# Optimization experiments

Hardware: AMD Instinct MI355X
Metric: run time of the kernel (lower is better)

## Reference

```python
import jax, jax.numpy as jnp
import numpy as np

# Classifier3Stage core of Reg_3stage (giga_depth), defaults: close_far_separation=False, c3_line_div=1
BS, CIN, H, W = 1, 128, 112, 320
CL = (16, 16, 16)          # classes per stage
PAD = (0, 8, 8)
C12 = CL[0] * CL[1]        # 256
C123 = C12 * CL[2]         # 4096
C1D = [128, 32, 32, CL[0] + 2 * PAD[0]]   # per-line grouped conv dims: 128->32->32->16
C2D = [128, 32, 32, CL[1] + 2 * PAD[1]]   # CondMul stage2 dims: 128->32->32->32
C3D = [128, 32, 32, CL[2] + 2 * PAD[2]]   # CondMul stage3 dims (in=ch_latent[0][i], out=ch_latent[1][i+1])


def setup_inputs() -> dict:
    key = jax.random.key(0)

    def p(i, shape):
        return jax.random.normal(jax.random.fold_in(key, i), shape, jnp.float32) * 0.05

    d = {"x_in": jax.random.normal(jax.random.fold_in(key, 0), (BS, CIN, H, W), jnp.float32)}
    for i in range(3):  # c1: per-line (grouped) 1x1 convs -> [H, out, in] weights
        d[f"w1_{i}"] = p(10 + 2 * i, (H, C1D[i + 1], C1D[i]))
        d[f"b1_{i}"] = p(11 + 2 * i, (H, C1D[i + 1]))
    for i in range(3):  # c2: CondMul over H*classes0 conditions
        d[f"w2_{i}"] = p(20 + 2 * i, (H * CL[0], C2D[i], C2D[i + 1]))
        d[f"b2_{i}"] = p(21 + 2 * i, (H * CL[0], C2D[i + 1]))
    for i in range(3):  # c3: CondMul over H*classes12 conditions
        d[f"w3_{i}"] = p(30 + 2 * i, (H * C12, C3D[i], C3D[i + 1]))
        d[f"b3_{i}"] = p(31 + 2 * i, (H * C12, C3D[i + 1]))
    return d


def _lrelu(v):
    return jnp.where(v >= 0, v, 0.01 * v)


def _condmul(x, inds, w, b):
    # x: [N, Cin], inds: [N] int32, w: [K, Cin, Cout], b: [K, Cout]
    return jnp.einsum('ni,nio->no', x, w[inds]) + b[inds]


def reference(x_in, w1_0, b1_0, w1_1, b1_1, w1_2, b1_2,
              w2_0, b2_0, w2_1, b2_1, w2_2, b2_2,
              w3_0, b3_0, w3_1, b3_1, w3_2, b3_2):
    bs, C, h, w = x_in.shape
    x = jnp.transpose(x_in, (0, 2, 3, 1))              # [bs,H,W,C] (far segment = x_in, per-line layout)
    # stage 1: per-line 1x1 grouped convs
    t = x
    for (wt, bt, last) in [(w1_0, b1_0, False), (w1_1, b1_1, False), (w1_2, b1_2, True)]:
        t = jnp.einsum('bhwi,hoi->bhwo', t, wt) + bt[None, :, None, :]
        if not last:
            t = _lrelu(t)
    inds1 = jnp.argmax(t, axis=-1).astype(jnp.int32)   # [bs,H,W]
    off = jnp.arange(h, dtype=jnp.int32)[None, :, None]
    x_l = x.reshape(-1, C)                             # rows in (b,h,w) order
    i1l = (inds1 + CL[0] * off).reshape(-1)
    # stage 2: CondMul chain routed by line*class1 index
    y = _lrelu(_condmul(x_l, i1l, w2_0, b2_0))
    y = _lrelu(_condmul(y, i1l, w2_1, b2_1))
    y = _condmul(y, i1l, w2_2, b2_2)                   # [N, 32]
    inds2 = jnp.argmax(y, axis=1).astype(jnp.int32).reshape(bs, h, w)
    inds12 = inds1 * CL[1] + (inds2 - PAD[1])
    i12l = (jnp.clip(inds12, 0, C12 - 1) + C12 * off).reshape(-1)  # c3_line_div=1 -> scaled == unscaled
    # stage 3: CondMul chain routed by line*classes12 index (close segment = x_in)
    z = _lrelu(_condmul(x_l, i12l, w3_0, b3_0))
    z = _lrelu(_condmul(z, i12l, w3_1, b3_1))
    z = _condmul(z, i12l, w3_2, b3_2)                  # [N, 32]
    inds3 = jnp.argmax(z, axis=1).astype(jnp.int32).reshape(bs, h, w)
    inds123 = jnp.clip(inds12 * CL[2] + (inds3 - PAD[2]), 0, C123 - 1)
    return inds123.reshape(bs, 1, h, w)
```

## Files before the change

### kernel.cpp

```cpp
#include <hip/hip_runtime.h>

#define HH   112
#define WW   320
#define CIN_ 128
#define HW_  (HH * WW)
#define CHUNK 32

__device__ __forceinline__ float lrelu(float v) {
    return v >= 0.f ? v : 0.01f * v;
}

__global__ __launch_bounds__(512, 2)
void k1_stage1(const float* __restrict__ x_in,
               const float* __restrict__ w1_0, const float* __restrict__ b1_0,
               const float* __restrict__ w1_1, const float* __restrict__ b1_1,
               const float* __restrict__ w1_2, const float* __restrict__ b1_2,
               int* __restrict__ inds1_out, float* __restrict__ xT_out,
               int* __restrict__ qc2, int* __restrict__ qc3)
{
    __shared__ float w1s0[32][CIN_ + 1];
    __shared__ float w1s1[32][33];
    __shared__ float w1s2[16][33];
    __shared__ float b1s[80];
    __shared__ float xT[16][132];

    const int h   = blockIdx.x >> 2;
    const int q   = blockIdx.x & 3;
    const int tid = threadIdx.x;
    const int base = h * WW;

    if (blockIdx.x == 0 && tid == 0) { *qc2 = 0; *qc3 = 0; }

    for (int n = tid; n < 32 * CIN_; n += 512)
        w1s0[n >> 7][n & 127] = w1_0[h * (32 * CIN_) + n];
    for (int n = tid; n < 32 * 32; n += 512)
        w1s1[n >> 5][n & 31] = w1_1[h * 1024 + n];
    if (tid < 16 * 32)
        w1s2[tid >> 5][tid & 31] = w1_2[h * 512 + tid];
    if      (tid < 32) b1s[tid] = b1_0[h * 32 + tid];
    else if (tid < 64) b1s[tid] = b1_1[h * 32 + (tid - 32)];
    else if (tid < 80) b1s[tid] = b1_2[h * 16 + (tid - 64)];
    __syncthreads();

    const int wave = tid >> 6;
    const int lane = tid & 63;
    const int o    = lane & 31;
    const int half = lane >> 5;
    const int o16  = lane & 15;

    for (int t = 0; t < 5; ++t) {
        const int w0 = q * 80 + t * 16;
        for (int n = tid; n < 16 * CIN_; n += 512) {
            int ww = n & 15, c = n >> 4;
            xT[ww][c] = x_in[c * HW_ + base + w0 + ww];
        }
        __syncthreads();
        for (int n = tid; n < 16 * CIN_; n += 512) {
            int pix = n >> 7, c = n & 127;
            xT_out[(size_t)(base + w0 + pix) * CIN_ + c] = xT[pix][c];
        }
        const float* xA = &xT[wave][0];
        const float* xB = &xT[wave + 8][0];

        float aA = 0.f, aB = 0.f;
        #pragma unroll
        for (int i = 0; i < 64; i += 4) {
            const int ii = half * 64 + i;
            const float w0v = w1s0[o][ii];
            const float w1v = w1s0[o][ii + 1];
            const float w2v = w1s0[o][ii + 2];
            const float w3v = w1s0[o][ii + 3];
            const float4 a4 = *reinterpret_cast<const float4*>(&xA[ii]);
            const float4 b4 = *reinterpret_cast<const float4*>(&xB[ii]);
            aA += a4.x * w0v;  aB += b4.x * w0v;
            aA += a4.y * w1v;  aB += b4.y * w1v;
            aA += a4.z * w2v;  aB += b4.z * w2v;
            aA += a4.w * w3v;  aB += b4.w * w3v;
        }
        aA += __shfl_xor(aA, 32);
        aB += __shfl_xor(aB, 32);
        float yA = lrelu(aA + b1s[o]);
        float yB = lrelu(aB + b1s[o]);

        aA = 0.f; aB = 0.f;
        #pragma unroll
        for (int i = 0; i < 32; ++i) {
            const float wv = w1s1[o][i];
            aA += __shfl(yA, i) * wv;
            aB += __shfl(yB, i) * wv;
        }
        float y2A = lrelu(aA + b1s[32 + o]);
        float y2B = lrelu(aB + b1s[32 + o]);

        aA = 0.f; aB = 0.f;
        #pragma unroll
        for (int i = 0; i < 32; ++i) {
            const float wv = w1s2[o16][i];
            aA += __shfl(y2A, i) * wv;
            aB += __shfl(y2B, i) * wv;
        }
        const float t1A = aA + b1s[64 + o16];
        const float t1B = aB + b1s[64 + o16];

        float bvA = t1A, bvB = t1B;
        int   biA = o16, biB = o16;
        #pragma unroll
        for (int d = 1; d < 16; d <<= 1) {
            float ovA = __shfl_xor(bvA, d), ovB = __shfl_xor(bvB, d);
            int   oiA = __shfl_xor(biA, d), oiB = __shfl_xor(biB, d);
            if (ovA > bvA || (ovA == bvA && oiA < biA)) { bvA = ovA; biA = oiA; }
            if (ovB > bvB || (ovB == bvB && oiB < biB)) { bvB = ovB; biB = oiB; }
        }
        if (lane == 0) {
            inds1_out[base + w0 + wave]     = biA;
            inds1_out[base + w0 + wave + 8] = biB;
        }
        __syncthreads();
    }
}

template <int BINS>
__global__ void sorter(const int* __restrict__ inds_in, int clipmax,
                       int* __restrict__ sorted, int4* __restrict__ queue,
                       int* __restrict__ qcount)
{
    __shared__ int cnt[BINS];
    __shared__ int scan[BINS];
    __shared__ int rank[BINS];

    const int h = blockIdx.x, tid = threadIdx.x, base = h * WW;
    if (tid < BINS) { cnt[tid] = 0; rank[tid] = 0; }
    __syncthreads();

    int c = -1;
    if (tid < WW) {
        c = inds_in[base + tid];
        c = min(max(c, 0), clipmax);
        atomicAdd(&cnt[c], 1);
    }
    __syncthreads();
    if (tid < BINS) scan[tid] = cnt[tid];
    __syncthreads();
    for (int s = 1; s < BINS; s <<= 1) {
        int v = 0;
        if (tid >= s && tid < BINS) v = scan[tid - s];
        __syncthreads();
        if (tid < BINS) scan[tid] += v;
        __syncthreads();
    }
    if (tid < WW) {
        int pos = (scan[c] - cnt[c]) + atomicAdd(&rank[c], 1);
        sorted[base + pos] = base + tid;
    }
    if (tid < BINS && cnt[tid] > 0) {
        int offc = scan[tid] - cnt[tid];
        for (int s0 = 0; s0 < cnt[tid]; s0 += CHUNK) {
            int qi = atomicAdd(qcount, 1);
            queue[qi] = make_int4(h, tid, base + offc + s0,
                                  min(CHUNK, cnt[tid] - s0));
        }
    }
}

#define COMPUTE_ROUND(TB, PA, PB, PC, PD)                                      \
{                                                                              \
    float a0 = 0.f, a1 = 0.f, a2 = 0.f, a3 = 0.f;                              \
    _Pragma("unroll")                                                          \
    for (int i = 0; i < 64; i += 4) {                                          \
        const int ii = half * 64 + i;                                          \
        const float w0v = ws0[(ii + 0) * 32 + o];                              \
        const float w1v = ws0[(ii + 1) * 32 + o];                              \
        const float w2v = ws0[(ii + 2) * 32 + o];                              \
        const float w3v = ws0[(ii + 3) * 32 + o];                              \
        const float4 v0 = *reinterpret_cast<const float4*>(&xbuf[wave*4+0][ii]);\
        const float4 v1 = *reinterpret_cast<const float4*>(&xbuf[wave*4+1][ii]);\
        const float4 v2 = *reinterpret_cast<const float4*>(&xbuf[wave*4+2][ii]);\
        const float4 v3 = *reinterpret_cast<const float4*>(&xbuf[wave*4+3][ii]);\
        a0 += v0.x * w0v; a1 += v1.x * w0v; a2 += v2.x * w0v; a3 += v3.x * w0v;\
        a0 += v0.y * w1v; a1 += v1.y * w1v; a2 += v2.y * w1v; a3 += v3.y * w1v;\
        a0 += v0.z * w2v; a1 += v1.z * w2v; a2 += v2.z * w2v; a3 += v3.z * w2v;\
        a0 += v0.w * w3v; a1 += v1.w * w3v; a2 += v2.w * w3v; a3 += v3.w * w3v;\
    }                                                                          \
    a0 += __shfl_xor(a0, 32); a1 += __shfl_xor(a1, 32);                        \
    a2 += __shfl_xor(a2, 32); a3 += __shfl_xor(a3, 32);                        \
    ys[wave][0][o] = lrelu(a0 + bs[o]);                                        \
    ys[wave][1][o] = lrelu(a1 + bs[o]);                                        \
    ys[wave][2][o] = lrelu(a2 + bs[o]);                                        \
    ys[wave][3][o] = lrelu(a3 + bs[o]);                                        \
    a0 = a1 = a2 = a3 = 0.f;                                                   \
    _Pragma("unroll")                                                          \
    for (int i = 0; i < 32; i += 4) {                                          \
        const float w0v = ws1[(i + 0) * 32 + o];                               \
        const float w1v = ws1[(i + 1) * 32 + o];                               \
        const float w2v = ws1[(i + 2) * 32 + o];                               \
        const float w3v = ws1[(i + 3) * 32 + o];                               \
        const float4 y0 = *reinterpret_cast<const float4*>(&ys[wave][0][i]);   \
        const float4 y1 = *reinterpret_cast<const float4*>(&ys[wave][1][i]);   \
        const float4 y2 = *reinterpret_cast<const float4*>(&ys[wave][2][i]);   \
        const float4 y3 = *reinterpret_cast<const float4*>(&ys[wave][3][i]);   \
        a0 += y0.x * w0v; a1 += y1.x * w0v; a2 += y2.x * w0v; a3 += y3.x * w0v;\
        a0 += y0.y * w1v; a1 += y1.y * w1v; a2 += y2.y * w1v; a3 += y3.y * w1v;\
        a0 += y0.z * w2v; a1 += y1.z * w2v; a2 += y2.z * w2v; a3 += y3.z * w2v;\
        a0 += y0.w * w3v; a1 += y1.w * w3v; a2 += y2.w * w3v; a3 += y3.w * w3v;\
    }                                                                          \
    ys[wave][0][o] = lrelu(a0 + bs[32 + o]);                                   \
    ys[wave][1][o] = lrelu(a1 + bs[32 + o]);                                   \
    ys[wave][2][o] = lrelu(a2 + bs[32 + o]);                                   \
    ys[wave][3][o] = lrelu(a3 + bs[32 + o]);                                   \
    a0 = a1 = a2 = a3 = 0.f;                                                   \
    _Pragma("unroll")                                                          \
    for (int i = 0; i < 32; i += 4) {                                          \
        const float w0v = ws2[(i + 0) * 32 + o];                               \
        const float w1v = ws2[(i + 1) * 32 + o];                               \
        const float w2v = ws2[(i + 2) * 32 + o];                               \
        const float w3v = ws2[(i + 3) * 32 + o];                               \
        const float4 y0 = *reinterpret_cast<const float4*>(&ys[wave][0][i]);   \
        const float4 y1 = *reinterpret_cast<const float4*>(&ys[wave][1][i]);   \
        const float4 y2 = *reinterpret_cast<const float4*>(&ys[wave][2][i]);   \
        const float4 y3 = *reinterpret_cast<const float4*>(&ys[wave][3][i]);   \
        a0 += y0.x * w0v; a1 += y1.x * w0v; a2 += y2.x * w0v; a3 += y3.x * w0v;\
        a0 += y0.y * w1v; a1 += y1.y * w1v; a2 += y2.y * w1v; a3 += y3.y * w1v;\
        a0 += y0.z * w2v; a1 += y1.z * w2v; a2 += y2.z * w2v; a3 += y3.z * w2v;\
        a0 += y0.w * w3v; a1 += y1.w * w3v; a2 += y2.w * w3v; a3 += y3.w * w3v;\
    }                                                                          \
    float bv0 = a0 + bs[64 + o], bv1 = a1 + bs[64 + o];                        \
    float bv2 = a2 + bs[64 + o], bv3 = a3 + bs[64 + o];                        \
    int bi0 = o, bi1 = o, bi2 = o, bi3 = o;                                    \
    _Pragma("unroll")                                                          \
    for (int d = 1; d < 32; d <<= 1) {                                         \
        const float ov0 = __shfl_xor(bv0, d); const int oi0 = __shfl_xor(bi0, d);\
        const float ov1 = __shfl_xor(bv1, d); const int oi1 = __shfl_xor(bi1, d);\
        const float ov2 = __shfl_xor(bv2, d); const int oi2 = __shfl_xor(bi2, d);\
        const float ov3 = __shfl_xor(bv3, d); const int oi3 = __shfl_xor(bi3, d);\
        if (ov0 > bv0 || (ov0 == bv0 && oi0 < bi0)) { bv0 = ov0; bi0 = oi0; }  \
        if (ov1 > bv1 || (ov1 == bv1 && oi1 < bi1)) { bv1 = ov1; bi1 = oi1; }  \
        if (ov2 > bv2 || (ov2 == bv2 && oi2 < bi2)) { bv2 = ov2; bi2 = oi2; }  \
        if (ov3 > bv3 || (ov3 == bv3 && oi3 < bi3)) { bv3 = ov3; bi3 = oi3; }  \
    }                                                                          \
    if (lane == 0) {                                                           \
        const int tb4 = (TB) + wave * 4;                                       \
        if (STAGE == 2) {                                                      \
            if (tb4 + 0 < n) result[PA] = c * 16 + bi0 - 8;                    \
            if (tb4 + 1 < n) result[PB] = c * 16 + bi1 - 8;                    \
            if (tb4 + 2 < n) result[PC] = c * 16 + bi2 - 8;                    \
            if (tb4 + 3 < n) result[PD] = c * 16 + bi3 - 8;                    \
        } else {                                                               \
            if (tb4 + 0 < n) result[PA] = min(max(inds12_in[PA] * 16 + bi0 - 8, 0), 4095); \
            if (tb4 + 1 < n) result[PB] = min(max(inds12_in[PB] * 16 + bi1 - 8, 0), 4095); \
            if (tb4 + 2 < n) result[PC] = min(max(inds12_in[PC] * 16 + bi2 - 8, 0), 4095); \
            if (tb4 + 3 < n) result[PD] = min(max(inds12_in[PD] * 16 + bi3 - 8, 0), 4095); \
        }                                                                      \
    }                                                                          \
}

template <int STAGE>
__global__ __launch_bounds__(256, 4)
void qk_compute(const float* __restrict__ xT_in, const int* __restrict__ sorted,
                const int4* __restrict__ queue, const int* __restrict__ qcount,
                const float* __restrict__ W0, const float* __restrict__ Bb0,
                const float* __restrict__ W1, const float* __restrict__ Bb1,
                const float* __restrict__ W2, const float* __restrict__ Bb2,
                const int* __restrict__ inds12_in, int* __restrict__ result)
{
    __shared__ float ws0[CIN_ * 32];
    __shared__ float ws1[32 * 32];
    __shared__ float ws2[32 * 32];
    __shared__ float bs[96];
    __shared__ float xbuf[16][CIN_];
    __shared__ float ys[4][4][32];

    const int tid  = threadIdx.x;
    const int wave = tid >> 6;
    const int lane = tid & 63;
    const int o    = lane & 31;
    const int half = lane >> 5;

    const int qn = *qcount;
    for (int qi = blockIdx.x; qi < qn; qi += gridDim.x) {
        const int4 it4   = queue[qi];
        const int  c     = it4.y;
        const int  start = it4.z;
        const int  n     = it4.w;
        const int  key   = (STAGE == 2) ? (it4.x * 16 + c) : (it4.x * 256 + c);
        const int  nr    = (n + 15) >> 4;
        const int  t0    = wave * 4;

        __syncthreads();

        const int pA0 = sorted[start + min(t0 + 0, n - 1)];
        const int pB0 = sorted[start + min(t0 + 1, n - 1)];
        const int pC0 = sorted[start + min(t0 + 2, n - 1)];
        const int pD0 = sorted[start + min(t0 + 3, n - 1)];
        const float2 xA0 = *reinterpret_cast<const float2*>(&xT_in[(size_t)pA0 * CIN_ + 2 * lane]);
        const float2 xB0 = *reinterpret_cast<const float2*>(&xT_in[(size_t)pB0 * CIN_ + 2 * lane]);
        const float2 xC0 = *reinterpret_cast<const float2*>(&xT_in[(size_t)pC0 * CIN_ + 2 * lane]);
        const float2 xD0 = *reinterpret_cast<const float2*>(&xT_in[(size_t)pD0 * CIN_ + 2 * lane]);

        for (int i = tid; i < 1024; i += 256)
            ((float4*)ws0)[i] = ((const float4*)(W0 + (size_t)key * 4096))[i];
        ((float4*)ws1)[tid] = ((const float4*)(W1 + (size_t)key * 1024))[tid];
        ((float4*)ws2)[tid] = ((const float4*)(W2 + (size_t)key * 1024))[tid];
        if      (tid < 32) bs[tid] = Bb0[(size_t)key * 32 + tid];
        else if (tid < 64) bs[tid] = Bb1[(size_t)key * 32 + (tid - 32)];
        else if (tid < 96) bs[tid] = Bb2[(size_t)key * 32 + (tid - 64)];
        __syncthreads();

        *reinterpret_cast<float2*>(&xbuf[wave * 4 + 0][2 * lane]) = xA0;
        *reinterpret_cast<float2*>(&xbuf[wave * 4 + 1][2 * lane]) = xB0;
        *reinterpret_cast<float2*>(&xbuf[wave * 4 + 2][2 * lane]) = xC0;
        *reinterpret_cast<float2*>(&xbuf[wave * 4 + 3][2 * lane]) = xD0;

        int pA1 = 0, pB1 = 0, pC1 = 0, pD1 = 0;
        float2 xA1 = {0.f, 0.f}, xB1 = {0.f, 0.f}, xC1 = {0.f, 0.f}, xD1 = {0.f, 0.f};
        if (nr == 2) {
            pA1 = sorted[start + min(16 + t0 + 0, n - 1)];
            pB1 = sorted[start + min(16 + t0 + 1, n - 1)];
            pC1 = sorted[start + min(16 + t0 + 2, n - 1)];
            pD1 = sorted[start + min(16 + t0 + 3, n - 1)];
            xA1 = *reinterpret_cast<const float2*>(&xT_in[(size_t)pA1 * CIN_ + 2 * lane]);
            xB1 = *reinterpret_cast<const float2*>(&xT_in[(size_t)pB1 * CIN_ + 2 * lane]);
            xC1 = *reinterpret_cast<const float2*>(&xT_in[(size_t)pC1 * CIN_ + 2 * lane]);
            xD1 = *reinterpret_cast<const float2*>(&xT_in[(size_t)pD1 * CIN_ + 2 * lane]);
        }

        COMPUTE_ROUND(0, pA0, pB0, pC0, pD0)

        if (nr == 2) {
            *reinterpret_cast<float2*>(&xbuf[wave * 4 + 0][2 * lane]) = xA1;
            *reinterpret_cast<float2*>(&xbuf[wave * 4 + 1][2 * lane]) = xB1;
            *reinterpret_cast<float2*>(&xbuf[wave * 4 + 2][2 * lane]) = xC1;
            *reinterpret_cast<float2*>(&xbuf[wave * 4 + 3][2 * lane]) = xD1;
            COMPUTE_ROUND(16, pA1, pB1, pC1, pD1)
        }
    }
}

__global__ __launch_bounds__(512, 4)
void reg3_fused(const float* __restrict__ x_in,
                const float* __restrict__ w1_0, const float* __restrict__ b1_0,
                const float* __restrict__ w1_1, const float* __restrict__ b1_1,
                const float* __restrict__ w1_2, const float* __restrict__ b1_2,
                const float* __restrict__ w2_0, const float* __restrict__ b2_0,
                const float* __restrict__ w2_1, const float* __restrict__ b2_1,
                const float* __restrict__ w2_2, const float* __restrict__ b2_2,
                const float* __restrict__ w3_0, const float* __restrict__ b3_0,
                const float* __restrict__ w3_1, const float* __restrict__ b3_1,
                const float* __restrict__ w3_2, const float* __restrict__ b3_2,
                int* __restrict__ out)
{
    __shared__ float xT[8][CIN_ + 1];
    __shared__ float w1s0[32][CIN_ + 1];
    __shared__ float w1s1[32][33];
    __shared__ float w1s2[16][33];
    __shared__ float b1s[80];

    const int h   = blockIdx.x / 40;
    const int w0  = (blockIdx.x % 40) * 8;
    const int tid = threadIdx.x;

    for (int n = tid; n < 8 * CIN_; n += 512) {
        int ww = n & 7, c = n >> 3;
        xT[ww][c] = x_in[c * HW_ + h * WW + w0 + ww];
    }
    for (int n = tid; n < 32 * CIN_; n += 512)
        w1s0[n >> 7][n & 127] = w1_0[h * (32 * CIN_) + n];
    for (int n = tid; n < 32 * 32; n += 512)
        w1s1[n >> 5][n & 31] = w1_1[h * 1024 + n];
    if (tid < 16 * 32)
        w1s2[tid >> 5][tid & 31] = w1_2[h * 512 + tid];
    if      (tid < 32) b1s[tid] = b1_0[h * 32 + tid];
    else if (tid < 64) b1s[tid] = b1_1[h * 32 + (tid - 32)];
    else if (tid < 80) b1s[tid] = b1_2[h * 16 + (tid - 64)];
    __syncthreads();

    const int wave = tid >> 6, lane = tid & 63;
    const int o = lane & 31, half = lane >> 5, o16 = lane & 15;
    const float* xr = &xT[wave][0];

    float acc = 0.f;
    #pragma unroll
    for (int i = 0; i < 64; ++i) { int ii = half * 64 + i; acc += xr[ii] * w1s0[o][ii]; }
    acc += __shfl_xor(acc, 32);
    float y = lrelu(acc + b1s[o]);
    acc = 0.f;
    #pragma unroll
    for (int i = 0; i < 32; ++i) acc += __shfl(y, i) * w1s1[o][i];
    float y2 = lrelu(acc + b1s[32 + o]);
    acc = 0.f;
    #pragma unroll
    for (int i = 0; i < 32; ++i) acc += __shfl(y2, i) * w1s2[o16][i];
    float t1 = acc + b1s[64 + o16];

    float bv = t1; int bi = o16;
    #pragma unroll
    for (int d = 1; d < 16; d <<= 1) {
        float ov = __shfl_xor(bv, d); int oi = __shfl_xor(bi, d);
        if (ov > bv || (ov == bv && oi < bi)) { bv = ov; bi = oi; }
    }
    const int inds1 = bi;
    const int idx1  = inds1 + 16 * h;

    const float* Wp = w2_0 + (size_t)idx1 * (CIN_ * 32);
    acc = 0.f;
    #pragma unroll
    for (int i = 0; i < 64; ++i) { int ii = half * 64 + i; acc += xr[ii] * Wp[ii * 32 + o]; }
    acc += __shfl_xor(acc, 32);
    y = lrelu(acc + b2_0[idx1 * 32 + o]);
    Wp = w2_1 + (size_t)idx1 * 1024;
    acc = 0.f;
    #pragma unroll
    for (int i = 0; i < 32; ++i) acc += __shfl(y, i) * Wp[i * 32 + o];
    y2 = lrelu(acc + b2_1[idx1 * 32 + o]);
    Wp = w2_2 + (size_t)idx1 * 1024;
    acc = 0.f;
    #pragma unroll
    for (int i = 0; i < 32; ++i) acc += __shfl(y2, i) * Wp[i * 32 + o];
    float y3 = acc + b2_2[idx1 * 32 + o];

    bv = y3; bi = o;
    #pragma unroll
    for (int d = 1; d < 32; d <<= 1) {
        float ov = __shfl_xor(bv, d); int oi = __shfl_xor(bi, d);
        if (ov > bv || (ov == bv && oi < bi)) { bv = ov; bi = oi; }
    }
    const int inds2  = bi;
    const int inds12 = inds1 * 16 + inds2 - 8;
    const int clip12 = min(max(inds12, 0), 255);
    const int idx12  = clip12 + 256 * h;

    Wp = w3_0 + (size_t)idx12 * (CIN_ * 32);
    acc = 0.f;
    #pragma unroll
    for (int i = 0; i < 64; ++i) { int ii = half * 64 + i; acc += xr[ii] * Wp[ii * 32 + o]; }
    acc += __shfl_xor(acc, 32);
    y = lrelu(acc + b3_0[idx12 * 32 + o]);
    Wp = w3_1 + (size_t)idx12 * 1024;
    acc = 0.f;
    #pragma unroll
    for (int i = 0; i < 32; ++i) acc += __shfl(y, i) * Wp[i * 32 + o];
    y2 = lrelu(acc + b3_1[idx12 * 32 + o]);
    Wp = w3_2 + (size_t)idx12 * 1024;
    acc = 0.f;
    #pragma unroll
    for (int i = 0; i < 32; ++i) acc += __shfl(y2, i) * Wp[i * 32 + o];
    y3 = acc + b3_2[idx12 * 32 + o];

    bv = y3; bi = o;
    #pragma unroll
    for (int d = 1; d < 32; d <<= 1) {
        float ov = __shfl_xor(bv, d); int oi = __shfl_xor(bi, d);
        if (ov > bv || (ov == bv && oi < bi)) { bv = ov; bi = oi; }
    }
    int inds123 = inds12 * 16 + bi - 8;
    inds123 = min(max(inds123, 0), 4095);
    if (lane == 0) out[h * WW + w0 + wave] = inds123;
}

extern "C" void kernel_launch(void* const* d_in, const int* in_sizes, int n_in,
                              void* d_out, int out_size, void* d_ws, size_t ws_size,
                              hipStream_t stream)
{
    const float* x_in = (const float*)d_in[0];
    const float* w1_0 = (const float*)d_in[1];
    const float* b1_0 = (const float*)d_in[2];
    const float* w1_1 = (const float*)d_in[3];
    const float* b1_1 = (const float*)d_in[4];
    const float* w1_2 = (const float*)d_in[5];
    const float* b1_2 = (const float*)d_in[6];
    const float* w2_0 = (const float*)d_in[7];
    const float* b2_0 = (const float*)d_in[8];
    const float* w2_1 = (const float*)d_in[9];
    const float* b2_1 = (const float*)d_in[10];
    const float* w2_2 = (const float*)d_in[11];
    const float* b2_2 = (const float*)d_in[12];
    const float* w3_0 = (const float*)d_in[13];
    const float* b3_0 = (const float*)d_in[14];
    const float* w3_1 = (const float*)d_in[15];
    const float* b3_1 = (const float*)d_in[16];
    const float* w3_2 = (const float*)d_in[17];
    const float* b3_2 = (const float*)d_in[18];
    int* out = (int*)d_out;

    char* ws = (char*)d_ws;
    int*   inds1_ws  = (int*)(ws + 0);
    int*   inds12_ws = (int*)(ws + 143360);
    int*   sorted2   = (int*)(ws + 286720);
    int*   sorted3   = (int*)(ws + 430080);
    int*   qc2       = (int*)(ws + 573440);
    int*   qc3       = (int*)(ws + 573444);
    int4*  queue2    = (int4*)(ws + 573456);
    int4*  queue3    = (int4*)(ws + 1146896);
    float* xT_ws     = (float*)(ws + 1720336);
    const size_t NEED = 1720336 + (size_t)HW_ * CIN_ * 4;

    if (ws_size >= NEED) {
        k1_stage1<<<HH * 4, 512, 0, stream>>>(
            x_in, w1_0, b1_0, w1_1, b1_1, w1_2, b1_2,
            inds1_ws, xT_ws, qc2, qc3);
        sorter<16><<<HH, 512, 0, stream>>>(inds1_ws, 15, sorted2, queue2, qc2);
        qk_compute<2><<<2048, 256, 0, stream>>>(
            xT_ws, sorted2, queue2, qc2,
            w2_0, b2_0, w2_1, b2_1, w2_2, b2_2, nullptr, inds12_ws);
        sorter<256><<<HH, 512, 0, stream>>>(inds12_ws, 255, sorted3, queue3, qc3);
        qk_compute<3><<<2048, 256, 0, stream>>>(
            xT_ws, sorted3, queue3, qc3,
            w3_0, b3_0, w3_1, b3_1, w3_2, b3_2, inds12_ws, out);
    } else {
        reg3_fused<<<HH * 40, 512, 0, stream>>>(
            x_in, w1_0, b1_0, w1_1, b1_1, w1_2, b1_2,
            w2_0, b2_0, w2_1, b2_1, w2_2, b2_2,
            w3_0, b3_0, w3_1, b3_1, w3_2, b3_2, out);
    }
}
```

Baseline: 200.0 us.

## Use single-wave work items reading condmul weights directly from global memory

The queue kernels now run one 64-thread wave per block with chunks of 8 pixels instead of 256-thread blocks with chunks of 32. Weights and biases are read straight from global memory (through cache) rather than staged in shared memory, which removes the block-wide barriers and the cost of staging a full weight set for small buckets. Per-item weight staging and barrier overhead go away, at the cost of more queue items and more global or L2 weight traffic when a bucket spans several chunks. The waitcnt plus sched_barrier stands in for the dropped __syncthreads, since each item is now handled by a single wave.

Result: slower. 231.1 us (+15.5%).

```diff
diff --git a/kernel.cpp b/kernel.cpp
--- a/kernel.cpp
+++ b/kernel.cpp
@@ -4,7 +4,7 @@
 #define WW   320
 #define CIN_ 128
 #define HW_  (HH * WW)
-#define CHUNK 32
+#define CHUNK 8
 
 __device__ __forceinline__ float lrelu(float v) {
     return v >= 0.f ? v : 0.01f * v;
@@ -162,20 +162,20 @@
     }
 }
 
-#define COMPUTE_ROUND(TB, PA, PB, PC, PD)                                      \
+#define COMPUTE_ROUND(TB, RB, PA, PB, PC, PD)                                  \
 {                                                                              \
     float a0 = 0.f, a1 = 0.f, a2 = 0.f, a3 = 0.f;                              \
     _Pragma("unroll")                                                          \
     for (int i = 0; i < 64; i += 4) {                                          \
         const int ii = half * 64 + i;                                          \
-        const float w0v = ws0[(ii + 0) * 32 + o];                              \
-        const float w1v = ws0[(ii + 1) * 32 + o];                              \
-        const float w2v = ws0[(ii + 2) * 32 + o];                              \
-        const float w3v = ws0[(ii + 3) * 32 + o];                              \
-        const float4 v0 = *reinterpret_cast<const float4*>(&xbuf[wave*4+0][ii]);\
-        const float4 v1 = *reinterpret_cast<const float4*>(&xbuf[wave*4+1][ii]);\
-        const float4 v2 = *reinterpret_cast<const float4*>(&xbuf[wave*4+2][ii]);\
-        const float4 v3 = *reinterpret_cast<const float4*>(&xbuf[wave*4+3][ii]);\
+        const float w0v = Wg0[(ii + 0) * 32 + o];                              \
+        const float w1v = Wg0[(ii + 1) * 32 + o];                              \
+        const float w2v = Wg0[(ii + 2) * 32 + o];                              \
+        const float w3v = Wg0[(ii + 3) * 32 + o];                              \
+        const float4 v0 = *reinterpret_cast<const float4*>(&xbuf[(RB) + 0][ii]);\
+        const float4 v1 = *reinterpret_cast<const float4*>(&xbuf[(RB) + 1][ii]);\
+        const float4 v2 = *reinterpret_cast<const float4*>(&xbuf[(RB) + 2][ii]);\
+        const float4 v3 = *reinterpret_cast<const float4*>(&xbuf[(RB) + 3][ii]);\
         a0 += v0.x * w0v; a1 += v1.x * w0v; a2 += v2.x * w0v; a3 += v3.x * w0v;\
         a0 += v0.y * w1v; a1 += v1.y * w1v; a2 += v2.y * w1v; a3 += v3.y * w1v;\
         a0 += v0.z * w2v; a1 += v1.z * w2v; a2 += v2.z * w2v; a3 += v3.z * w2v;\
@@ -183,48 +183,48 @@
     }                                                                          \
     a0 += __shfl_xor(a0, 32); a1 += __shfl_xor(a1, 32);                        \
     a2 += __shfl_xor(a2, 32); a3 += __shfl_xor(a3, 32);                        \
-    ys[wave][0][o] = lrelu(a0 + bs[o]);                                        \
-    ys[wave][1][o] = lrelu(a1 + bs[o]);                                        \
-    ys[wave][2][o] = lrelu(a2 + bs[o]);                                        \
-    ys[wave][3][o] = lrelu(a3 + bs[o]);                                        \
+    ys[0][o] = lrelu(a0 + b0v);                                                \
+    ys[1][o] = lrelu(a1 + b0v);                                                \
+    ys[2][o] = lrelu(a2 + b0v);                                                \
+    ys[3][o] = lrelu(a3 + b0v);                                                \
     a0 = a1 = a2 = a3 = 0.f;                                                   \
     _Pragma("unroll")                                                          \
     for (int i = 0; i < 32; i += 4) {                                          \
-        const float w0v = ws1[(i + 0) * 32 + o];                               \
-        const float w1v = ws1[(i + 1) * 32 + o];                               \
-        const float w2v = ws1[(i + 2) * 32 + o];                               \
-        const float w3v = ws1[(i + 3) * 32 + o];                               \
-        const float4 y0 = *reinterpret_cast<const float4*>(&ys[wave][0][i]);   \
-        const float4 y1 = *reinterpret_cast<const float4*>(&ys[wave][1][i]);   \
-        const float4 y2 = *reinterpret_cast<const float4*>(&ys[wave][2][i]);   \
-        const float4 y3 = *reinterpret_cast<const float4*>(&ys[wave][3][i]);   \
+        const float w0v = Wg1[(i + 0) * 32 + o];                               \
+        const float w1v = Wg1[(i + 1) * 32 + o];                               \
+        const float w2v = Wg1[(i + 2) * 32 + o];                               \
+        const float w3v = Wg1[(i + 3) * 32 + o];                               \
+        const float4 y0 = *reinterpret_cast<const float4*>(&ys[0][i]);         \
+        const float4 y1 = *reinterpret_cast<const float4*>(&ys[1][i]);         \
+        const float4 y2 = *reinterpret_cast<const float4*>(&ys[2][i]);         \
+        const float4 y3 = *reinterpret_cast<const float4*>(&ys[3][i]);         \
         a0 += y0.x * w0v; a1 += y1.x * w0v; a2 += y2.x * w0v; a3 += y3.x * w0v;\
         a0 += y0.y * w1v; a1 += y1.y * w1v; a2 += y2.y * w1v; a3 += y3.y * w1v;\
         a0 += y0.z * w2v; a1 += y1.z * w2v; a2 += y2.z * w2v; a3 += y3.z * w2v;\
         a0 += y0.w * w3v; a1 += y1.w * w3v; a2 += y2.w * w3v; a3 += y3.w * w3v;\
     }                                                                          \
-    ys[wave][0][o] = lrelu(a0 + bs[32 + o]);                                   \
-    ys[wave][1][o] = lrelu(a1 + bs[32 + o]);                                   \
-    ys[wave][2][o] = lrelu(a2 + bs[32 + o]);                                   \
-    ys[wave][3][o] = lrelu(a3 + bs[32 + o]);                                   \
+    ys[0][o] = lrelu(a0 + b1v);                                                \
+    ys[1][o] = lrelu(a1 + b1v);                                                \
+    ys[2][o] = lrelu(a2 + b1v);                                                \
+    ys[3][o] = lrelu(a3 + b1v);                                                \
     a0 = a1 = a2 = a3 = 0.f;                                                   \
     _Pragma("unroll")                                                          \
     for (int i = 0; i < 32; i += 4) {                                          \
-        const float w0v = ws2[(i + 0) * 32 + o];                               \
-        const float w1v = ws2[(i + 1) * 32 + o];                               \
-        const float w2v = ws2[(i + 2) * 32 + o];                               \
-        const float w3v = ws2[(i + 3) * 32 + o];                               \
-        const float4 y0 = *reinterpret_cast<const float4*>(&ys[wave][0][i]);   \
-        const float4 y1 = *reinterpret_cast<const float4*>(&ys[wave][1][i]);   \
-        const float4 y2 = *reinterpret_cast<const float4*>(&ys[wave][2][i]);   \
-        const float4 y3 = *reinterpret_cast<const float4*>(&ys[wave][3][i]);   \
+        const float w0v = Wg2[(i + 0) * 32 + o];                               \
+        const float w1v = Wg2[(i + 1) * 32 + o];                               \
+        const float w2v = Wg2[(i + 2) * 32 + o];                               \
+        const float w3v = Wg2[(i + 3) * 32 + o];                               \
+        const float4 y0 = *reinterpret_cast<const float4*>(&ys[0][i]);         \
+        const float4 y1 = *reinterpret_cast<const float4*>(&ys[1][i]);         \
+        const float4 y2 = *reinterpret_cast<const float4*>(&ys[2][i]);         \
+        const float4 y3 = *reinterpret_cast<const float4*>(&ys[3][i]);         \
         a0 += y0.x * w0v; a1 += y1.x * w0v; a2 += y2.x * w0v; a3 += y3.x * w0v;\
         a0 += y0.y * w1v; a1 += y1.y * w1v; a2 += y2.y * w1v; a3 += y3.y * w1v;\
         a0 += y0.z * w2v; a1 += y1.z * w2v; a2 += y2.z * w2v; a3 += y3.z * w2v;\
         a0 += y0.w * w3v; a1 += y1.w * w3v; a2 += y2.w * w3v; a3 += y3.w * w3v;\
     }                                                                          \
-    float bv0 = a0 + bs[64 + o], bv1 = a1 + bs[64 + o];                        \
-    float bv2 = a2 + bs[64 + o], bv3 = a3 + bs[64 + o];                        \
+    float bv0 = a0 + b2v, bv1 = a1 + b2v;                                      \
+    float bv2 = a2 + b2v, bv3 = a3 + b2v;                                      \
     int bi0 = o, bi1 = o, bi2 = o, bi3 = o;                                    \
     _Pragma("unroll")                                                          \
     for (int d = 1; d < 32; d <<= 1) {                                         \
@@ -238,23 +238,22 @@
         if (ov3 > bv3 || (ov3 == bv3 && oi3 < bi3)) { bv3 = ov3; bi3 = oi3; }  \
     }                                                                          \
     if (lane == 0) {                                                           \
-        const int tb4 = (TB) + wave * 4;                                       \
         if (STAGE == 2) {                                                      \
-            if (tb4 + 0 < n) result[PA] = c * 16 + bi0 - 8;                    \
-            if (tb4 + 1 < n) result[PB] = c * 16 + bi1 - 8;                    \
-            if (tb4 + 2 < n) result[PC] = c * 16 + bi2 - 8;                    \
-            if (tb4 + 3 < n) result[PD] = c * 16 + bi3 - 8;                    \
+            if ((TB) + 0 < n) result[PA] = c * 16 + bi0 - 8;                   \
+            if ((TB) + 1 < n) result[PB] = c * 16 + bi1 - 8;                   \
+            if ((TB) + 2 < n) result[PC] = c * 16 + bi2 - 8;                   \
+            if ((TB) + 3 < n) result[PD] = c * 16 + bi3 - 8;                   \
         } else {                                                               \
-            if (tb4 + 0 < n) result[PA] = min(max(inds12_in[PA] * 16 + bi0 - 8, 0), 4095); \
-            if (tb4 + 1 < n) result[PB] = min(max(inds12_in[PB] * 16 + bi1 - 8, 0), 4095); \
-            if (tb4 + 2 < n) result[PC] = min(max(inds12_in[PC] * 16 + bi2 - 8, 0), 4095); \
-            if (tb4 + 3 < n) result[PD] = min(max(inds12_in[PD] * 16 + bi3 - 8, 0), 4095); \
+            if ((TB) + 0 < n) result[PA] = min(max(inds12_in[PA] * 16 + bi0 - 8, 0), 4095); \
+            if ((TB) + 1 < n) result[PB] = min(max(inds12_in[PB] * 16 + bi1 - 8, 0), 4095); \
+            if ((TB) + 2 < n) result[PC] = min(max(inds12_in[PC] * 16 + bi2 - 8, 0), 4095); \
+            if ((TB) + 3 < n) result[PD] = min(max(inds12_in[PD] * 16 + bi3 - 8, 0), 4095); \
         }                                                                      \
     }                                                                          \
 }
 
 template <int STAGE>
-__global__ __launch_bounds__(256, 4)
+__global__ __launch_bounds__(64, 4)
 void qk_compute(const float* __restrict__ xT_in, const int* __restrict__ sorted,
                 const int4* __restrict__ queue, const int* __restrict__ qcount,
                 const float* __restrict__ W0, const float* __restrict__ Bb0,
@@ -262,16 +261,10 @@
                 const float* __restrict__ W2, const float* __restrict__ Bb2,
                 const int* __restrict__ inds12_in, int* __restrict__ result)
 {
-    __shared__ float ws0[CIN_ * 32];
-    __shared__ float ws1[32 * 32];
-    __shared__ float ws2[32 * 32];
-    __shared__ float bs[96];
-    __shared__ float xbuf[16][CIN_];
-    __shared__ float ys[4][4][32];
-
-    const int tid  = threadIdx.x;
-    const int wave = tid >> 6;
-    const int lane = tid & 63;
+    __shared__ float xbuf[8][CIN_];
+    __shared__ float ys[4][32];
+
+    const int lane = threadIdx.x;
     const int o    = lane & 31;
     const int half = lane >> 5;
 
@@ -282,55 +275,45 @@
         const int  start = it4.z;
         const int  n     = it4.w;
         const int  key   = (STAGE == 2) ? (it4.x * 16 + c) : (it4.x * 256 + c);
-        const int  nr    = (n + 15) >> 4;
-        const int  t0    = wave * 4;
-
-        __syncthreads();
-
-        const int pA0 = sorted[start + min(t0 + 0, n - 1)];
-        const int pB0 = sorted[start + min(t0 + 1, n - 1)];
-        const int pC0 = sorted[start + min(t0 + 2, n - 1)];
-        const int pD0 = sorted[start + min(t0 + 3, n - 1)];
+
+        const float* __restrict__ Wg0 = W0 + (size_t)key * 4096;
+        const float* __restrict__ Wg1 = W1 + (size_t)key * 1024;
+        const float* __restrict__ Wg2 = W2 + (size_t)key * 1024;
+        const float b0v = Bb0[(size_t)key * 32 + o];
+        const float b1v = Bb1[(size_t)key * 32 + o];
+        const float b2v = Bb2[(size_t)key * 32 + o];
+
+        const int pA0 = sorted[start + min(0, n - 1)];
+        const int pB0 = sorted[start + min(1, n - 1)];
+        const int pC0 = sorted[start + min(2, n - 1)];
+        const int pD0 = sorted[start + min(3, n - 1)];
+        const int pA1 = sorted[start + min(4, n - 1)];
+        const int pB1 = sorted[start + min(5, n - 1)];
+        const int pC1 = sorted[start + min(6, n - 1)];
+        const int pD1 = sorted[start + min(7, n - 1)];
         const float2 xA0 = *reinterpret_cast<const float2*>(&xT_in[(size_t)pA0 * CIN_ + 2 * lane]);
         const float2 xB0 = *reinterpret_cast<const float2*>(&xT_in[(size_t)pB0 * CIN_ + 2 * lane]);
         const float2 xC0 = *reinterpret_cast<const float2*>(&xT_in[(size_t)pC0 * CIN_ + 2 * lane]);
         const float2 xD0 = *reinterpret_cast<const float2*>(&xT_in[(size_t)pD0 * CIN_ + 2 * lane]);
-
-        for (int i = tid; i < 1024; i += 256)
-            ((float4*)ws0)[i] = ((const float4*)(W0 + (size_t)key * 4096))[i];
-        ((float4*)ws1)[tid] = ((const float4*)(W1 + (size_t)key * 1024))[tid];
-        ((float4*)ws2)[tid] = ((const float4*)(W2 + (size_t)key * 1024))[tid];
-        if      (tid < 32) bs[tid] = Bb0[(size_t)key * 32 + tid];
-        else if (tid < 64) bs[tid] = Bb1[(size_t)key * 32 + (tid - 32)];
-        else if (tid < 96) bs[tid] = Bb2[(size_t)key * 32 + (tid - 64)];
-        __syncthreads();
-
-        *reinterpret_cast<float2*>(&xbuf[wave * 4 + 0][2 * lane]) = xA0;
-        *reinterpret_cast<float2*>(&xbuf[wave * 4 + 1][2 * lane]) = xB0;
-        *reinterpret_cast<float2*>(&xbuf[wave * 4 + 2][2 * lane]) = xC0;
-        *reinterpret_cast<float2*>(&xbuf[wave * 4 + 3][2 * lane]) = xD0;
-
-        int pA1 = 0, pB1 = 0, pC1 = 0, pD1 = 0;
-        float2 xA1 = {0.f, 0.f}, xB1 = {0.f, 0.f}, xC1 = {0.f, 0.f}, xD1 = {0.f, 0.f};
-        if (nr == 2) {
-            pA1 = sorted[start + min(16 + t0 + 0, n - 1)];
-            pB1 = sorted[start + min(16 + t0 + 1, n - 1)];
-            pC1 = sorted[start + min(16 + t0 + 2, n - 1)];
-            pD1 = sorted[start + min(16 + t0 + 3, n - 1)];
-            xA1 = *reinterpret_cast<const float2*>(&xT_in[(size_t)pA1 * CIN_ + 2 * lane]);
-            xB1 = *reinterpret_cast<const float2*>(&xT_in[(size_t)pB1 * CIN_ + 2 * lane]);
-            xC1 = *reinterpret_cast<const float2*>(&xT_in[(size_t)pC1 * CIN_ + 2 * lane]);
-            xD1 = *reinterpret_cast<const float2*>(&xT_in[(size_t)pD1 * CIN_ + 2 * lane]);
-        }
-
-        COMPUTE_ROUND(0, pA0, pB0, pC0, pD0)
-
-        if (nr == 2) {
-            *reinterpret_cast<float2*>(&xbuf[wave * 4 + 0][2 * lane]) = xA1;
-            *reinterpret_cast<float2*>(&xbuf[wave * 4 + 1][2 * lane]) = xB1;
-            *reinterpret_cast<float2*>(&xbuf[wave * 4 + 2][2 * lane]) = xC1;
-            *reinterpret_cast<float2*>(&xbuf[wave * 4 + 3][2 * lane]) = xD1;
-            COMPUTE_ROUND(16, pA1, pB1, pC1, pD1)
+        const float2 xA1 = *reinterpret_cast<const float2*>(&xT_in[(size_t)pA1 * CIN_ + 2 * lane]);
+        const float2 xB1 = *reinterpret_cast<const float2*>(&xT_in[(size_t)pB1 * CIN_ + 2 * lane]);
+        const float2 xC1 = *reinterpret_cast<const float2*>(&xT_in[(size_t)pC1 * CIN_ + 2 * lane]);
+        const float2 xD1 = *reinterpret_cast<const float2*>(&xT_in[(size_t)pD1 * CIN_ + 2 * lane]);
+        *reinterpret_cast<float2*>(&xbuf[0][2 * lane]) = xA0;
+        *reinterpret_cast<float2*>(&xbuf[1][2 * lane]) = xB0;
+        *reinterpret_cast<float2*>(&xbuf[2][2 * lane]) = xC0;
+        *reinterpret_cast<float2*>(&xbuf[3][2 * lane]) = xD0;
+        *reinterpret_cast<float2*>(&xbuf[4][2 * lane]) = xA1;
+        *reinterpret_cast<float2*>(&xbuf[5][2 * lane]) = xB1;
+        *reinterpret_cast<float2*>(&xbuf[6][2 * lane]) = xC1;
+        *reinterpret_cast<float2*>(&xbuf[7][2 * lane]) = xD1;
+        asm volatile("s_waitcnt lgkmcnt(0)" ::: "memory");
+        __builtin_amdgcn_sched_barrier(0);
+
+        COMPUTE_ROUND(0, 0, pA0, pB0, pC0, pD0)
+
+        if (n > 4) {
+            COMPUTE_ROUND(4, 4, pA1, pB1, pC1, pD1)
         }
     }
 }
@@ -498,11 +481,11 @@
             x_in, w1_0, b1_0, w1_1, b1_1, w1_2, b1_2,
             inds1_ws, xT_ws, qc2, qc3);
         sorter<16><<<HH, 512, 0, stream>>>(inds1_ws, 15, sorted2, queue2, qc2);
-        qk_compute<2><<<2048, 256, 0, stream>>>(
+        qk_compute<2><<<8192, 64, 0, stream>>>(
             xT_ws, sorted2, queue2, qc2,
             w2_0, b2_0, w2_1, b2_1, w2_2, b2_2, nullptr, inds12_ws);
         sorter<256><<<HH, 512, 0, stream>>>(inds12_ws, 255, sorted3, queue3, qc3);
-        qk_compute<3><<<2048, 256, 0, stream>>>(
+        qk_compute<3><<<8192, 64, 0, stream>>>(
             xT_ws, sorted3, queue3, qc3,
             w3_0, b3_0, w3_1, b3_1, w3_2, b3_2, inds12_ws, out);
     } else {
```
